# Kernel optimization log

Measured on AMD Instinct MI355X. Metric: run time of the kernel, lower is better.

Reference implementation:

```python
import jax, jax.numpy as jnp
import numpy as np

IN_DIM = 128
HIDDEN = 128


def setup_inputs() -> dict:
    key = jax.random.key(0)
    k1, k2, k3, k4, k5 = jax.random.split(key, 5)
    bound_ih = 1.0 / np.sqrt(IN_DIM)
    bound_hh = 1.0 / np.sqrt(HIDDEN)
    return {
        "x": jax.random.normal(k1, (256, 2048, IN_DIM), dtype=jnp.float32),
        "W_ih": jax.random.uniform(k2, (HIDDEN, IN_DIM), minval=-bound_ih, maxval=bound_ih, dtype=jnp.float32),
        "b_ih": jax.random.uniform(k3, (HIDDEN,), minval=-bound_ih, maxval=bound_ih, dtype=jnp.float32),
        "W_hh": jax.random.uniform(k4, (HIDDEN, HIDDEN), minval=-bound_hh, maxval=bound_hh, dtype=jnp.float32),
        "b_hh": jax.random.uniform(k5, (HIDDEN,), minval=-bound_hh, maxval=bound_hh, dtype=jnp.float32),
    }


def reference(x, W_ih, b_ih, W_hh, b_hh):
    B, S, _ = x.shape
    # Precompute input projection for all timesteps in one big GEMM: [B,S,H]
    xw = jnp.einsum("bsi,hi->bsh", x, W_ih) + b_ih
    h0 = jnp.zeros((B, W_hh.shape[0]), dtype=x.dtype)

    def step(h, xw_t):
        h_new = jnp.tanh(xw_t + h @ W_hh.T + b_hh)
        return h_new, None

    # scan over time axis: move S to leading dim
    h_final, _ = jax.lax.scan(step, h0, jnp.swapaxes(xw, 0, 1))
    return h_final
```

## Files before the change

### kernel.cpp

```cpp
#include <hip/hip_runtime.h>


#define BATCH 256
#define SEQ   2048
#define HID   128
#define CH    16
#define NCHUNK (SEQ / CH)

typedef __attribute__((ext_vector_type(8))) short bf16x8;
typedef __attribute__((ext_vector_type(4))) float f32x4;

template <int CTRL>
__device__ __forceinline__ float dpp_movf(float x) {
    return __int_as_float(__builtin_amdgcn_mov_dpp(__float_as_int(x), CTRL, 0xF, 0xF, true));
}

__device__ __forceinline__ float tanh_fast(float x) {
    x = fminf(fmaxf(x, -12.0f), 12.0f);
    float e = __expf(2.0f * x);
    return 1.0f - __fdividef(2.0f, e + 1.0f);
}

__device__ __forceinline__ void bf16_split(float v, short& hi, short& lo) {
    unsigned u = __float_as_uint(v);
    unsigned hb = (u + 0x8000u) & 0xFFFF0000u;
    float hf = __uint_as_float(hb);
    float r = v - hf;
    unsigned ru = __float_as_uint(r);
    hi = (short)(hb >> 16);
    lo = (short)((ru + 0x8000u) >> 16);
}

__global__ __launch_bounds__(512, 2) void rnn_scan_kernel(
    const float* __restrict__ x,
    const float* __restrict__ Wih,
    const float* __restrict__ bih,
    const float* __restrict__ Whh,
    const float* __restrict__ bhh,
    float* __restrict__ out)
{
    const int b = blockIdx.x;
    const int t = threadIdx.x;
    const int g = t >> 4;
    const int c = t & 15;
    const int colbase = c << 3;
    const int rowbase = g << 2;
    const int lane = t & 63;
    const int w = t >> 6;

    __shared__ __align__(16) ushort xbf[2][2][CH * HID];
    __shared__ __align__(16) float  xwbuf[2][CH * HID];
    __shared__ __align__(16) float  hbuf[2][192];

    float4 wh[4][2];
#pragma unroll
    for (int r = 0; r < 4; ++r) {
        const float* ph = Whh + (rowbase + r) * HID + colbase;
        wh[r][0] = *(const float4*)(ph);
        wh[r][1] = *(const float4*)(ph + 4);
    }

    const int bcol = (w << 4) + (lane & 15);
    const int krow = (lane >> 4) << 3;
    bf16x8 bhi[4], blo[4];
#pragma unroll
    for (int kk = 0; kk < 4; ++kk) {
        const float* src = Wih + bcol * HID + kk * 32 + krow;
        float4 u0 = *(const float4*)(src);
        float4 u1 = *(const float4*)(src + 4);
        short hh, ll;
        bf16_split(u0.x, hh, ll); bhi[kk][0] = hh; blo[kk][0] = ll;
        bf16_split(u0.y, hh, ll); bhi[kk][1] = hh; blo[kk][1] = ll;
        bf16_split(u0.z, hh, ll); bhi[kk][2] = hh; blo[kk][2] = ll;
        bf16_split(u0.w, hh, ll); bhi[kk][3] = hh; blo[kk][3] = ll;
        bf16_split(u1.x, hh, ll); bhi[kk][4] = hh; blo[kk][4] = ll;
        bf16_split(u1.y, hh, ll); bhi[kk][5] = hh; blo[kk][5] = ll;
        bf16_split(u1.z, hh, ll); bhi[kk][6] = hh; blo[kk][6] = ll;
        bf16_split(u1.w, hh, ll); bhi[kk][7] = hh; blo[kk][7] = ll;
    }

    const int m = c & 3;
    const int o = ((m & 1) << 1) | ((m >> 1) & 1);
    const int row0 = rowbase + o;
    const float bias = bih[row0] + bhh[row0];
    const int hw = row0 + ((row0 >> 3) << 2);

    const float* xsrc = x + (size_t)b * (SEQ * HID);

    auto stage_bf16 = [&](float4 q, int buf) {
        const int srow = t >> 5;
        const int sw = ((srow << 8) + ((t & 31) << 3)) ^ ((srow & 7) << 4);
        short h0, l0, h1, l1, h2, l2, h3, l3;
        bf16_split(q.x, h0, l0); bf16_split(q.y, h1, l1);
        bf16_split(q.z, h2, l2); bf16_split(q.w, h3, l3);
        uint2 ph, pl;
        ph.x = (unsigned)(ushort)h0 | ((unsigned)(ushort)h1 << 16);
        ph.y = (unsigned)(ushort)h2 | ((unsigned)(ushort)h3 << 16);
        pl.x = (unsigned)(ushort)l0 | ((unsigned)(ushort)l1 << 16);
        pl.y = (unsigned)(ushort)l2 | ((unsigned)(ushort)l3 << 16);
        *(uint2*)((char*)&xbf[buf][0][0] + sw) = ph;
        *(uint2*)((char*)&xbf[buf][1][0] + sw) = pl;
    };

    auto compute_xw = [&](int mm) {
        const int buf = mm & 1;
        const int arow = lane & 15;
        const int rowb = (arow << 8) + ((lane >> 4) << 4);
        const int swz = (arow & 7) << 4;
        const char* hp = (const char*)&xbf[buf][0][0];
        const char* lp = (const char*)&xbf[buf][1][0];
        f32x4 acc0 = {0.0f, 0.0f, 0.0f, 0.0f};
        f32x4 acc1 = {0.0f, 0.0f, 0.0f, 0.0f};
#pragma unroll
        for (int kk = 0; kk < 4; ++kk) {
            const int off = (rowb + kk * 64) ^ swz;
            bf16x8 ah = *(const bf16x8*)(hp + off);
            bf16x8 al = *(const bf16x8*)(lp + off);
            f32x4& acc = (kk & 1) ? acc1 : acc0;
            acc = __builtin_amdgcn_mfma_f32_16x16x32_bf16(ah, bhi[kk], acc, 0, 0, 0);
            acc = __builtin_amdgcn_mfma_f32_16x16x32_bf16(ah, blo[kk], acc, 0, 0, 0);
            acc = __builtin_amdgcn_mfma_f32_16x16x32_bf16(al, bhi[kk], acc, 0, 0, 0);
        }
        float* xw = &xwbuf[buf][0];
        const int crow = (lane >> 4) << 2;
#pragma unroll
        for (int r = 0; r < 4; ++r) xw[(crow + r) * HID + bcol] = acc0[r] + acc1[r];
    };

    {
        const float4* gp = (const float4*)xsrc;
        float4 a0 = gp[t];
        float4 a1 = gp[512 + t];
        stage_bf16(a0, 0);
        stage_bf16(a1, 1);
    }
    if (t < 192) hbuf[0][t] = 0.0f;
    __syncthreads();
    compute_xw(0);
    __syncthreads();

    int cur = 0;
    for (int n = 0; n < NCHUNK; ++n) {
        float4 q0;
        const bool pf = (n + 2 < NCHUNK);
        if (pf) {
            const float4* gp = (const float4*)(xsrc + (size_t)(n + 2) * (CH * HID));
            q0 = gp[t];
        }
        const float* xwc = &xwbuf[n & 1][0];
#pragma unroll 1
        for (int s = 0; s < CH; ++s) {
            float xwv = 0.0f;
            if (c < 4) xwv = xwc[s * HID + row0];
            const float* hr = &hbuf[cur][12 * c];
            float4 hv0 = *(const float4*)(hr);
            float4 hv1 = *(const float4*)(hr + 4);

            float a[4];
#pragma unroll
            for (int r = 0; r < 4; ++r) {
                float acc;
                acc = wh[r][0].x * hv0.x;
                acc = fmaf(wh[r][0].y, hv0.y, acc);
                acc = fmaf(wh[r][0].z, hv0.z, acc);
                acc = fmaf(wh[r][0].w, hv0.w, acc);
                acc = fmaf(wh[r][1].x, hv1.x, acc);
                acc = fmaf(wh[r][1].y, hv1.y, acc);
                acc = fmaf(wh[r][1].z, hv1.z, acc);
                acc = fmaf(wh[r][1].w, hv1.w, acc);
                a[r] = acc;
            }

            const bool b0 = (c & 1) != 0;
            const bool b1 = (c & 2) != 0;
            float k0 = b0 ? a[2] : a[0], s0 = b0 ? a[0] : a[2];
            float k1 = b0 ? a[3] : a[1], s1 = b0 ? a[1] : a[3];
            float t0 = k0 + dpp_movf<0xB1>(s0);
            float t1 = k1 + dpp_movf<0xB1>(s1);
            float k2 = b1 ? t1 : t0, s2 = b1 ? t0 : t1;
            float u = k2 + dpp_movf<0x4E>(s2);
            u += dpp_movf<0x124>(u);
            u += dpp_movf<0x128>(u);

            float hval = tanh_fast(u + bias + xwv);
            if (c < 4) {
                hbuf[cur ^ 1][hw] = hval;
            }

            if (s == 0 && n + 1 < NCHUNK) compute_xw(n + 1);
            if (s == CH - 1 && pf) stage_bf16(q0, n & 1);

            __syncthreads();
            cur ^= 1;
        }
    }
    if (t < HID) out[(size_t)b * HID + t] = hbuf[cur][t + ((t >> 3) << 2)];
}

extern "C" void kernel_launch(void* const* d_in, const int* in_sizes, int n_in,
                              void* d_out, int out_size, void* d_ws, size_t ws_size,
                              hipStream_t stream) {
    const float* x   = (const float*)d_in[0];
    const float* Wih = (const float*)d_in[1];
    const float* bih = (const float*)d_in[2];
    const float* Whh = (const float*)d_in[3];
    const float* bhh = (const float*)d_in[4];
    float* out = (float*)d_out;

    rnn_scan_kernel<<<BATCH, 512, 0, stream>>>(x, Wih, bih, Whh, bhh, out);
}
```

Before: 1.082 ms.

## Double block to 1024 threads, two hidden rows per 16-lane group

Each block now uses 1024 threads, and each 16-lane group computes two rows of W_hh·h instead of four. This halves the per-thread FMA chain and shortens the cross-lane DPP reduction on the serial recurrence critical path. The input-projection MFMA and staging work is restricted to the first 8 warps or 512 threads, and the combined bias is folded into the xw buffer. The cost is more waves synchronising at every per-step barrier and possibly lower occupancy from the larger block size.

```diff
diff --git a/kernel.cpp b/kernel.cpp
--- a/kernel.cpp
+++ b/kernel.cpp
@@ -31,7 +31,7 @@
     lo = (short)((ru + 0x8000u) >> 16);
 }
 
-__global__ __launch_bounds__(512, 2) void rnn_scan_kernel(
+__global__ __launch_bounds__(1024, 4) void rnn_scan_kernel(
     const float* __restrict__ x,
     const float* __restrict__ Wih,
     const float* __restrict__ bih,
@@ -44,7 +44,7 @@
     const int g = t >> 4;
     const int c = t & 15;
     const int colbase = c << 3;
-    const int rowbase = g << 2;
+    const int rowbase = g << 1;
     const int lane = t & 63;
     const int w = t >> 6;
 
@@ -52,44 +52,44 @@
     __shared__ __align__(16) float  xwbuf[2][CH * HID];
     __shared__ __align__(16) float  hbuf[2][192];
 
-    float4 wh[4][2];
-#pragma unroll
-    for (int r = 0; r < 4; ++r) {
+    float4 wh[2][2];
+#pragma unroll
+    for (int r = 0; r < 2; ++r) {
         const float* ph = Whh + (rowbase + r) * HID + colbase;
         wh[r][0] = *(const float4*)(ph);
         wh[r][1] = *(const float4*)(ph + 4);
     }
 
-    const int bcol = (w << 4) + (lane & 15);
-    const int krow = (lane >> 4) << 3;
+    const int bcol = ((w & 7) << 4) + (lane & 15);
     bf16x8 bhi[4], blo[4];
-#pragma unroll
-    for (int kk = 0; kk < 4; ++kk) {
-        const float* src = Wih + bcol * HID + kk * 32 + krow;
-        float4 u0 = *(const float4*)(src);
-        float4 u1 = *(const float4*)(src + 4);
-        short hh, ll;
-        bf16_split(u0.x, hh, ll); bhi[kk][0] = hh; blo[kk][0] = ll;
-        bf16_split(u0.y, hh, ll); bhi[kk][1] = hh; blo[kk][1] = ll;
-        bf16_split(u0.z, hh, ll); bhi[kk][2] = hh; blo[kk][2] = ll;
-        bf16_split(u0.w, hh, ll); bhi[kk][3] = hh; blo[kk][3] = ll;
-        bf16_split(u1.x, hh, ll); bhi[kk][4] = hh; blo[kk][4] = ll;
-        bf16_split(u1.y, hh, ll); bhi[kk][5] = hh; blo[kk][5] = ll;
-        bf16_split(u1.z, hh, ll); bhi[kk][6] = hh; blo[kk][6] = ll;
-        bf16_split(u1.w, hh, ll); bhi[kk][7] = hh; blo[kk][7] = ll;
-    }
-
-    const int m = c & 3;
-    const int o = ((m & 1) << 1) | ((m >> 1) & 1);
-    const int row0 = rowbase + o;
-    const float bias = bih[row0] + bhh[row0];
+    float biasv = 0.0f;
+    if (w < 8) {
+        biasv = bih[bcol] + bhh[bcol];
+#pragma unroll
+        for (int kk = 0; kk < 4; ++kk) {
+            const float* src = Wih + bcol * HID + kk * 32 + ((lane >> 4) << 3);
+            float4 u0 = *(const float4*)(src);
+            float4 u1 = *(const float4*)(src + 4);
+            short hh, ll;
+            bf16_split(u0.x, hh, ll); bhi[kk][0] = hh; blo[kk][0] = ll;
+            bf16_split(u0.y, hh, ll); bhi[kk][1] = hh; blo[kk][1] = ll;
+            bf16_split(u0.z, hh, ll); bhi[kk][2] = hh; blo[kk][2] = ll;
+            bf16_split(u0.w, hh, ll); bhi[kk][3] = hh; blo[kk][3] = ll;
+            bf16_split(u1.x, hh, ll); bhi[kk][4] = hh; blo[kk][4] = ll;
+            bf16_split(u1.y, hh, ll); bhi[kk][5] = hh; blo[kk][5] = ll;
+            bf16_split(u1.z, hh, ll); bhi[kk][6] = hh; blo[kk][6] = ll;
+            bf16_split(u1.w, hh, ll); bhi[kk][7] = hh; blo[kk][7] = ll;
+        }
+    }
+
+    const int row0 = rowbase + (c & 1);
     const int hw = row0 + ((row0 >> 3) << 2);
 
     const float* xsrc = x + (size_t)b * (SEQ * HID);
 
-    auto stage_bf16 = [&](float4 q, int buf) {
-        const int srow = t >> 5;
-        const int sw = ((srow << 8) + ((t & 31) << 3)) ^ ((srow & 7) << 4);
+    auto stage_bf16 = [&](float4 q, int buf, int idx) {
+        const int srow = idx >> 5;
+        const int sw = ((srow << 8) + ((idx & 31) << 3)) ^ ((srow & 7) << 4);
         short h0, l0, h1, l1, h2, l2, h3, l3;
         bf16_split(q.x, h0, l0); bf16_split(q.y, h1, l1);
         bf16_split(q.z, h2, l2); bf16_split(q.w, h3, l3);
@@ -124,71 +124,72 @@
         float* xw = &xwbuf[buf][0];
         const int crow = (lane >> 4) << 2;
 #pragma unroll
-        for (int r = 0; r < 4; ++r) xw[(crow + r) * HID + bcol] = acc0[r] + acc1[r];
+        for (int r = 0; r < 4; ++r)
+            xw[(crow + r) * HID + bcol] = acc0[r] + acc1[r] + biasv;
     };
 
     {
         const float4* gp = (const float4*)xsrc;
-        float4 a0 = gp[t];
-        float4 a1 = gp[512 + t];
-        stage_bf16(a0, 0);
-        stage_bf16(a1, 1);
+        stage_bf16(gp[t], t >> 9, t & 511);
     }
     if (t < 192) hbuf[0][t] = 0.0f;
     __syncthreads();
-    compute_xw(0);
+    if (w < 8) compute_xw(0);
     __syncthreads();
 
     int cur = 0;
     for (int n = 0; n < NCHUNK; ++n) {
         float4 q0;
         const bool pf = (n + 2 < NCHUNK);
-        if (pf) {
+        if (pf && t < 512) {
             const float4* gp = (const float4*)(xsrc + (size_t)(n + 2) * (CH * HID));
             q0 = gp[t];
         }
         const float* xwc = &xwbuf[n & 1][0];
 #pragma unroll 1
         for (int s = 0; s < CH; ++s) {
-            float xwv = 0.0f;
-            if (c < 4) xwv = xwc[s * HID + row0];
+            float xwv = xwc[s * HID + row0];
             const float* hr = &hbuf[cur][12 * c];
             float4 hv0 = *(const float4*)(hr);
             float4 hv1 = *(const float4*)(hr + 4);
 
-            float a[4];
-#pragma unroll
-            for (int r = 0; r < 4; ++r) {
+            float a0, a1;
+            {
                 float acc;
-                acc = wh[r][0].x * hv0.x;
-                acc = fmaf(wh[r][0].y, hv0.y, acc);
-                acc = fmaf(wh[r][0].z, hv0.z, acc);
-                acc = fmaf(wh[r][0].w, hv0.w, acc);
-                acc = fmaf(wh[r][1].x, hv1.x, acc);
-                acc = fmaf(wh[r][1].y, hv1.y, acc);
-                acc = fmaf(wh[r][1].z, hv1.z, acc);
-                acc = fmaf(wh[r][1].w, hv1.w, acc);
-                a[r] = acc;
+                acc = wh[0][0].x * hv0.x;
+                acc = fmaf(wh[0][0].y, hv0.y, acc);
+                acc = fmaf(wh[0][0].z, hv0.z, acc);
+                acc = fmaf(wh[0][0].w, hv0.w, acc);
+                acc = fmaf(wh[0][1].x, hv1.x, acc);
+                acc = fmaf(wh[0][1].y, hv1.y, acc);
+                acc = fmaf(wh[0][1].z, hv1.z, acc);
+                acc = fmaf(wh[0][1].w, hv1.w, acc);
+                a0 = acc;
+                acc = wh[1][0].x * hv0.x;
+                acc = fmaf(wh[1][0].y, hv0.y, acc);
+                acc = fmaf(wh[1][0].z, hv0.z, acc);
+                acc = fmaf(wh[1][0].w, hv0.w, acc);
+                acc = fmaf(wh[1][1].x, hv1.x, acc);
+                acc = fmaf(wh[1][1].y, hv1.y, acc);
+                acc = fmaf(wh[1][1].z, hv1.z, acc);
+                acc = fmaf(wh[1][1].w, hv1.w, acc);
+                a1 = acc;
             }
 
             const bool b0 = (c & 1) != 0;
-            const bool b1 = (c & 2) != 0;
-            float k0 = b0 ? a[2] : a[0], s0 = b0 ? a[0] : a[2];
-            float k1 = b0 ? a[3] : a[1], s1 = b0 ? a[1] : a[3];
-            float t0 = k0 + dpp_movf<0xB1>(s0);
-            float t1 = k1 + dpp_movf<0xB1>(s1);
-            float k2 = b1 ? t1 : t0, s2 = b1 ? t0 : t1;
-            float u = k2 + dpp_movf<0x4E>(s2);
+            float k0 = b0 ? a1 : a0, s0 = b0 ? a0 : a1;
+            float u = k0 + dpp_movf<0xB1>(s0);
+            u += dpp_movf<0x4E>(u);
             u += dpp_movf<0x124>(u);
             u += dpp_movf<0x128>(u);
 
-            float hval = tanh_fast(u + bias + xwv);
-            if (c < 4) {
+            float hval = tanh_fast(u + xwv);
+            if (c < 2) {
                 hbuf[cur ^ 1][hw] = hval;
             }
 
-            if (s == 0 && n + 1 < NCHUNK) compute_xw(n + 1);
-            if (s == CH - 1 && pf) stage_bf16(q0, n & 1);
+            if (s == 0 && n + 1 < NCHUNK && w < 8) compute_xw(n + 1);
+            if (s == CH - 1 && pf && t < 512) stage_bf16(q0, n & 1, t);
 
             __syncthreads();
             cur ^= 1;
@@ -207,5 +208,5 @@
     const float* bhh = (const float*)d_in[4];
     float* out = (float*)d_out;
 
-    rnn_scan_kernel<<<BATCH, 512, 0, stream>>>(x, Wih, bih, Whh, bhh, out);
-}
+    rnn_scan_kernel<<<BATCH, 1024, 0, stream>>>(x, Wih, bih, Whh, bhh, out);
+}
```

Result: slower. 1.203 ms (+11.1%).
